# Performance work log

Hardware: AMD Instinct MI355X
Metric: run time of the kernel (lower is better)

The kernel has to match this reference:

```python
import jax, jax.numpy as jnp
import numpy as np

N, E, F, H, G, C = 50000, 800000, 128, 128, 500, 10
L = 3  # num_conv_layers
EPS = 1e-5


def batch_norm(x, g, b):
    # training-mode BatchNorm1d: biased variance, eps=1e-5
    mu = jnp.mean(x, axis=0)
    var = jnp.var(x, axis=0)
    return (x - mu) * jax.lax.rsqrt(var + EPS) * g + b


def gcn_conv(x, W, bias, src, dst, n):
    # x' = D^{-1/2} (A + I) D^{-1/2} (x W) + bias, edge weights = 1
    xw = x @ W
    loop = jnp.arange(n)
    s = jnp.concatenate([src, loop])  # sources incl. self-loops
    d = jnp.concatenate([dst, loop])  # targets incl. self-loops
    w = jnp.ones(s.shape[0], x.dtype)
    deg = jax.ops.segment_sum(w, s, num_segments=n)
    dinv = jnp.where(deg > 0, jax.lax.rsqrt(deg), 0.0)
    norm = dinv[s] * w * dinv[d]
    msg = xw[s] * norm[:, None]  # gather + scale
    out = jax.ops.segment_sum(msg, d, num_segments=n)  # scatter-add
    return out + bias


def setup_inputs() -> dict:
    key = jax.random.key(0)
    ks = jax.random.split(key, 16)
    x = jax.random.normal(ks[0], (N, F), dtype=jnp.float32)
    edge_index = jax.random.randint(ks[1], (2, E), 0, N, dtype=jnp.int64)
    batch = jnp.sort(jax.random.randint(ks[2], (N,), 0, G, dtype=jnp.int64))
    sF = 1.0 / np.sqrt(F)
    sH = 1.0 / np.sqrt(H)
    return {
        "x": x,
        "edge_index": edge_index,
        "batch": batch,
        "bn_feat_g": jnp.ones((F,), jnp.float32),
        "bn_feat_b": jnp.full((F,), 1e-4, jnp.float32),
        "W_feat": jax.random.normal(ks[3], (F, H), jnp.float32) * sF,
        "bns_conv_g": jnp.ones((L, H), jnp.float32),
        "bns_conv_b": jnp.full((L, H), 1e-4, jnp.float32),
        "W_conv": jax.random.normal(ks[4], (L, H, H), jnp.float32) * sH,
        "b_conv": jnp.zeros((L, H), jnp.float32),
        "bn_fc_g": jnp.ones((H,), jnp.float32),
        "bn_fc_b": jnp.full((H,), 1e-4, jnp.float32),
        "W_lin": jax.random.normal(ks[5], (H, H), jnp.float32) * sH,
        "b_lin": jnp.zeros((H,), jnp.float32),
        "bn_hid_g": jnp.ones((H,), jnp.float32),
        "bn_hid_b": jnp.full((H,), 1e-4, jnp.float32),
        "W_cls": jax.random.normal(ks[6], (H, C), jnp.float32) * sH,
        "b_cls": jnp.zeros((C,), jnp.float32),
    }


def reference(x, edge_index, batch, bn_feat_g, bn_feat_b, W_feat,
              bns_conv_g, bns_conv_b, W_conv, b_conv,
              bn_fc_g, bn_fc_b, W_lin, b_lin,
              bn_hid_g, bn_hid_b, W_cls, b_cls):
    src, dst = edge_index[0], edge_index[1]
    h = batch_norm(x, bn_feat_g, bn_feat_b)
    h = jax.nn.relu(h @ W_feat)  # gfn conv: linear only, no bias/propagation
    for i in range(L):
        h = batch_norm(h, bns_conv_g[i], bns_conv_b[i])
        h = jax.nn.relu(gcn_conv(h, W_conv[i], b_conv[i], src, dst, N))
    h = jax.ops.segment_sum(h, batch, num_segments=G)  # global_add_pool
    h = batch_norm(h, bn_fc_g, bn_fc_b)
    h = jax.nn.relu(h @ W_lin + b_lin)
    h = batch_norm(h, bn_hid_g, bn_hid_b)
    logits = h @ W_cls + b_cls
    return jax.nn.log_softmax(logits, axis=-1)
```

## Files before the change

### kernel.cpp

```cpp
#include <hip/hip_runtime.h>

#define NF 128
#define EPS 1e-5f
#define KELL 64
#define HB 64
#define HRANGE 32768
#define BCAP 5120
#define SB 512

typedef unsigned short ushort_t;
typedef unsigned int uint_t;

using bf16x8 = __attribute__((ext_vector_type(8))) short;
using f32x4  = __attribute__((ext_vector_type(4))) float;

static __device__ inline ushort_t f2bf(float f) {
    uint_t u = __float_as_uint(f);
    return (ushort_t)((u + 0x7fffu + ((u >> 16) & 1u)) >> 16);
}


__launch_bounds__(1024)
__global__ void k_prep(const int* __restrict__ ei, uint_t* __restrict__ gcnt,
                       uint_t* __restrict__ bedge, uint_t* __restrict__ hpart,
                       const float* __restrict__ W0, const float* __restrict__ W123,
                       ushort_t* __restrict__ Wp, const float* __restrict__ x,
                       float* __restrict__ stx, int E, int n) {
    __shared__ union {
        struct { uint_t cnt[256]; uint_t cur[256]; uint_t base[256]; } bk;
        uint_t h2[HRANGE / 2];
        struct { float ls[1024]; float lq[1024]; } st;
    } sh;
    const int blk = blockIdx.x;
    const int t = threadIdx.x;

    if (blk < 256) {
        if (t < 256) { sh.bk.cnt[t] = 0; sh.bk.cur[t] = 0; }
        __syncthreads();
        const int chunk = (E + 255) / 256;
        const int e0 = blk * chunk;
        const int e1 = min(e0 + chunk, E);
        for (int e = e0 + t; e < e1; e += 1024)
            atomicAdd(&sh.bk.cnt[ei[E + e] >> 8], 1);
        __syncthreads();
        if (t < 256) {
            uint_t c = sh.bk.cnt[t];
            sh.bk.base[t] = c ? atomicAdd(&gcnt[t], c) : 0u;
        }
        __syncthreads();
        for (int e = e0 + t; e < e1; e += 1024) {
            int s = ei[e], d = ei[E + e];
            int b = d >> 8;
            uint_t pos = sh.bk.base[b] + atomicAdd(&sh.bk.cur[b], 1);
            if (pos < BCAP)
                bedge[((size_t)b << 12) + ((size_t)b << 10) + pos] =
                    ((uint_t)(d & 255) << 16) | (uint_t)s;
        }
    } else if (blk < 320) {
        const int b = blk - 256;
#pragma unroll
        for (int p = 0; p < 2; ++p) {
            int base = p * HRANGE;
            for (int w = t; w < HRANGE / 2; w += 1024) sh.h2[w] = 0;
            __syncthreads();
            for (int e = b * 1024 + t; e < E; e += HB * 1024) {
                unsigned u = (unsigned)(ei[e] - base);
                if (u < HRANGE)
                    atomicAdd(&sh.h2[u >> 1], 1u << ((u & 1) << 4));
            }
            __syncthreads();
            uint_t* dst = hpart + ((size_t)(p * HB + b) << 14);
            for (int w = t; w < HRANGE / 2; w += 1024) dst[w] = sh.h2[w];
            __syncthreads();
        }
    } else if (blk < 322) {
#pragma unroll
        for (int kk = 0; kk < 4; ++kk) {
            int gidx = (blk - 320) * 4096 + kk * 1024 + t;
            int mat = gidx >> 11, idx = gidx & 2047;
            const float* W = (mat == 0) ? W0 : (W123 + (size_t)(mat - 1) * NF * NF);
            int lane = idx & 63, ct = (idx >> 6) & 7, kc = idx >> 9;
            int m = lane & 15, q = lane >> 4;
            ushort_t o[8];
#pragma unroll
            for (int j = 0; j < 8; ++j)
                o[j] = f2bf(W[(kc * 32 + q * 8 + j) * NF + ct * 16 + m]);
            *(uint4*)&Wp[(size_t)gidx * 8] = *(uint4*)o;
        }
    } else {
        const int b = blk - 322;
        const int j = t & 127;
        const int row8 = t >> 7;
        float s = 0.f, q = 0.f;
        for (int r = b * 8 + row8; r < n; r += SB * 8) {
            float v = x[(size_t)r * NF + j];
            s += v; q += v * v;
        }
        sh.st.ls[t] = s; sh.st.lq[t] = q;
        __syncthreads();
        if (t < 128) {
            float ss = 0.f, qq = 0.f;
#pragma unroll
            for (int k = 0; k < 8; ++k) {
                ss += sh.st.ls[t + k * 128];
                qq += sh.st.lq[t + k * 128];
            }
            atomicAdd(&stx[t], ss);
            atomicAdd(&stx[NF + t], qq);
        }
    }
}

__launch_bounds__(256)
__global__ void k_build(const uint_t* __restrict__ gcnt, const uint_t* __restrict__ bedge,
                        const uint_t* __restrict__ hpart, int* __restrict__ ucnt,
                        float* __restrict__ dinv, ushort_t* __restrict__ colx,
                        ushort_t* __restrict__ BbSent, int n) {
    __shared__ ushort_t ell[256][KELL];
    __shared__ uint_t lcnt[256];
    const int b = blockIdx.x, t = threadIdx.x;
    lcnt[t] = 0;
    __syncthreads();
    const int nb = min((int)gcnt[b], BCAP);
    const int node0 = b << 8;
    const uint_t* bsrc = bedge + ((size_t)b << 12) + ((size_t)b << 10);
    for (int e = t; e < nb; e += 256) {
        uint_t pk = bsrc[e];
        int dl = (pk >> 16) & 255;
        uint_t pos = atomicAdd(&lcnt[dl], 1);
        if (pos < KELL - 1) ell[dl][pos] = (ushort_t)(pk & 0xffffu);
    }
    __syncthreads();
    const int i = node0 + t;
    if (i < n) {
        int w = min((int)lcnt[t], KELL - 1);
        ell[t][w] = (ushort_t)i;
        int len = (w + 16) & ~15;
        for (int q = w + 1; q < len; ++q) ell[t][q] = (ushort_t)n;
        ucnt[i] = w;
        int p = i >> 15;
        int u = i & (HRANGE - 1);
        int wd = u >> 1, sh = (u & 1) << 4;
        const uint_t* basep = hpart + ((size_t)(p * HB) << 14) + wd;
        uint_t sum = 0;
#pragma unroll 8
        for (int bb = 0; bb < HB; ++bb) sum += basep[(size_t)bb << 14];
        sum = (sum >> sh) & 0xffffu;
        dinv[i] = rsqrtf((float)sum + 1.0f);
    }
    __syncthreads();
    int nrow = min(n - node0, 256);
    if (nrow > 0) {
        const uint4* src = (const uint4*)&ell[0][0];
        uint4* dst = (uint4*)&colx[(size_t)node0 * KELL];
        int lim = nrow * (KELL * 2 / 16);
        for (int wds = t; wds < lim; wds += 256) dst[wds] = src[wds];
    }
    if (b == 0 && t < 64)
        ((uint_t*)BbSent)[t] = 0;
}


__global__ void bn_stats_bf(const ushort_t* __restrict__ h, float* __restrict__ stats, int n) {
    int j = threadIdx.x & 127;
    int half = threadIdx.x >> 7;
    float s = 0.f, q = 0.f;
    for (int r = blockIdx.x * 2 + half; r < n; r += gridDim.x * 2) {
        float v = __uint_as_float((uint_t)h[(size_t)r * NF + j] << 16);
        s += v;
        q += v * v;
    }
    __shared__ float ls[256], lq[256];
    ls[threadIdx.x] = s; lq[threadIdx.x] = q;
    __syncthreads();
    if (threadIdx.x < 128) {
        atomicAdd(&stats[j], ls[threadIdx.x] + ls[threadIdx.x + 128]);
        atomicAdd(&stats[NF + j], lq[threadIdx.x] + lq[threadIdx.x + 128]);
    }
}


#define HSTRIDE 136

__launch_bounds__(512)
__global__ void gemm_mfma(const void* __restrict__ In, int inbf, const ushort_t* __restrict__ Wp,
                          const float* __restrict__ stats, const float* __restrict__ gW,
                          const float* __restrict__ bB, float inv_n,
                          const float* __restrict__ bias, const float* __restrict__ rowscale,
                          float* __restrict__ out, ushort_t* __restrict__ outb,
                          float* __restrict__ statsOut,
                          int nrows, int relu, int obf) {
    __shared__ union {
        ushort_t hs[64 * HSTRIDE];
        float    ob[32][132];
        ushort_t obu[64][136];
    } shu;
    __shared__ float acs[256];
    __shared__ float cs[128], cq[128];
    const int tid = threadIdx.x;
    const int rb = blockIdx.x * 64;

    if (tid < 128) {
        float mean = stats[tid] * inv_n;
        float var = stats[NF + tid] * inv_n - mean * mean;
        float rstd = rsqrtf(var + EPS);
        float a = gW[tid] * rstd;
        acs[tid] = a;
        acs[NF + tid] = bB[tid] - mean * a;
        cs[tid] = 0.f; cq[tid] = 0.f;
    }
    __syncthreads();
    const float4* ac4 = (const float4*)acs;

#pragma unroll
    for (int p = 0; p < 4; ++p) {
        int idx = p * 512 + tid;
        int r = idx >> 5, k4 = idx & 31;
        int gr = rb + r;
        float4 v = make_float4(0.f, 0.f, 0.f, 0.f);
        if (gr < nrows) {
            if (inbf) {
                uint2 u = *(const uint2*)((const ushort_t*)In + (size_t)gr * NF + k4 * 4);
                v.x = __uint_as_float(u.x << 16);
                v.y = __uint_as_float(u.x & 0xffff0000u);
                v.z = __uint_as_float(u.y << 16);
                v.w = __uint_as_float(u.y & 0xffff0000u);
            } else {
                v = *(const float4*)((const float*)In + (size_t)gr * NF + k4 * 4);
            }
        }
        float4 a4 = ac4[k4], c4 = ac4[32 + k4];
        ushort_t o[4];
        o[0] = f2bf(fmaf(v.x, a4.x, c4.x));
        o[1] = f2bf(fmaf(v.y, a4.y, c4.y));
        o[2] = f2bf(fmaf(v.z, a4.z, c4.z));
        o[3] = f2bf(fmaf(v.w, a4.w, c4.w));
        *(uint2*)&shu.hs[r * HSTRIDE + k4 * 4] = *(uint2*)o;
    }
    __syncthreads();

    const int wave = tid >> 6, lane = tid & 63;
    const int wr = wave & 3;
    const int wc = wave >> 2;
    const int m = lane & 15, q = lane >> 4;
    const ushort_t* arow = &shu.hs[(wr * 16 + m) * HSTRIDE];

    f32x4 acc[4];
#pragma unroll
    for (int ct = 0; ct < 4; ++ct) acc[ct] = (f32x4){0.f, 0.f, 0.f, 0.f};

#pragma unroll
    for (int kc = 0; kc < 4; ++kc) {
        bf16x8 af = *(const bf16x8*)&arow[kc * 32 + q * 8];
        const ushort_t* wp = Wp + kc * 4096 + (wc * 4) * 512 + lane * 8;
#pragma unroll
        for (int ct = 0; ct < 4; ++ct) {
            bf16x8 bfr = *(const bf16x8*)&wp[ct * 512];
            acc[ct] = __builtin_amdgcn_mfma_f32_16x16x32_bf16(af, bfr, acc[ct], 0, 0, 0);
        }
    }

    int grows[4]; float rsv[4]; bool gv[4];
#pragma unroll
    for (int r = 0; r < 4; ++r) {
        grows[r] = rb + wr * 16 + q * 4 + r;
        gv[r] = grows[r] < nrows;
        rsv[r] = (obf && rowscale && gv[r]) ? rowscale[grows[r]] : 1.0f;
    }

    if (statsOut) {
#pragma unroll
        for (int ct = 0; ct < 4; ++ct) {
            int col = (wc * 4 + ct) * 16 + m;
            float bcol = bias ? bias[col] : 0.f;
            float s = 0.f, qq = 0.f;
#pragma unroll
            for (int r = 0; r < 4; ++r) {
                if (gv[r]) {
                    float v = acc[ct][r] + bcol;
                    if (relu) v = fmaxf(v, 0.f);
                    s += v; qq += v * v;
                }
            }
            atomicAdd(&cs[col], s); atomicAdd(&cq[col], qq);
        }
    }

    __syncthreads();

    if (obf) {
#pragma unroll
        for (int ct = 0; ct < 4; ++ct) {
            int col = (wc * 4 + ct) * 16 + m;
            float bcol = bias ? bias[col] : 0.f;
#pragma unroll
            for (int r = 0; r < 4; ++r) {
                int row = wr * 16 + q * 4 + r;
                float v = acc[ct][r] + bcol;
                if (relu) v = fmaxf(v, 0.f);
                shu.obu[row][col] = f2bf(v * rsv[r]);
            }
        }
        __syncthreads();
#pragma unroll
        for (int i = 0; i < 2; ++i) {
            int idx = i * 512 + tid;
            int r = idx >> 4, c8 = idx & 15;
            int grow = rb + r;
            if (grow < nrows)
                *(uint4*)&outb[(size_t)grow * NF + c8 * 8] =
                    *(const uint4*)&shu.obu[r][c8 * 8];
        }
    } else {
#pragma unroll
        for (int h = 0; h < 2; ++h) {
            if ((wr >> 1) == h) {
#pragma unroll
                for (int ct = 0; ct < 4; ++ct) {
                    int col = (wc * 4 + ct) * 16 + m;
                    float bcol = bias ? bias[col] : 0.f;
#pragma unroll
                    for (int r = 0; r < 4; ++r) {
                        int row = (wr & 1) * 16 + q * 4 + r;
                        float v = acc[ct][r] + bcol;
                        if (relu) v = fmaxf(v, 0.f);
                        shu.ob[row][col] = v;
                    }
                }
            }
            __syncthreads();
#pragma unroll
            for (int i = 0; i < 2; ++i) {
                int idx = i * 512 + tid;
                int r = idx >> 5, c4 = idx & 31;
                int grow = rb + h * 32 + r;
                if (grow < nrows)
                    *(float4*)&out[(size_t)grow * NF + c4 * 4] =
                        *(const float4*)&shu.ob[r][c4 * 4];
            }
            __syncthreads();
        }
    }

    if (statsOut) {
        if (tid < 128) {
            atomicAdd(&statsOut[tid], cs[tid]);
            atomicAdd(&statsOut[NF + tid], cq[tid]);
        }
    }
}


__launch_bounds__(256)
__global__ void gemm_bn(const float* __restrict__ Hh, const float* __restrict__ W,
                        const float* __restrict__ stats, const float* __restrict__ gW,
                        const float* __restrict__ bB, float inv_n,
                        const float* __restrict__ bias,
                        float* __restrict__ out, float* __restrict__ statsOut,
                        int nrows, int relu) {
    __shared__ float hsb[64][133];
    __shared__ float acs[256];
    __shared__ float cs[128], cq[128];
    const int tid = threadIdx.x;
    const int tx = tid & 15;
    const int ty = tid >> 4;
    const int rb = blockIdx.x * 64;

    if (tid < 128) {
        float mean = stats[tid] * inv_n;
        float var = stats[NF + tid] * inv_n - mean * mean;
        float rstd = rsqrtf(var + EPS);
        float a = gW[tid] * rstd;
        acs[tid] = a;
        acs[NF + tid] = bB[tid] - mean * a;
        cs[tid] = 0.f; cq[tid] = 0.f;
    }
    __syncthreads();

#pragma unroll 8
    for (int p = 0; p < 32; ++p) {
        int idx = p * 256 + tid;
        int r = idx >> 7, k = idx & 127;
        int gr = rb + r;
        float v = (gr < nrows) ? Hh[(size_t)gr * NF + k] : 0.f;
        hsb[r][k] = fmaf(v, acs[k], acs[NF + k]);
    }
    __syncthreads();

    float acc[4][8];
#pragma unroll
    for (int i = 0; i < 4; ++i)
#pragma unroll
        for (int j = 0; j < 8; ++j) acc[i][j] = 0.f;

    const int c0 = tx * 4, c1 = 64 + tx * 4;
#pragma unroll 4
    for (int k = 0; k < 128; ++k) {
        const float4 b0 = *(const float4*)&W[k * NF + c0];
        const float4 b1 = *(const float4*)&W[k * NF + c1];
#pragma unroll
        for (int i = 0; i < 4; ++i) {
            float a = hsb[ty * 4 + i][k];
            acc[i][0] = fmaf(a, b0.x, acc[i][0]);
            acc[i][1] = fmaf(a, b0.y, acc[i][1]);
            acc[i][2] = fmaf(a, b0.z, acc[i][2]);
            acc[i][3] = fmaf(a, b0.w, acc[i][3]);
            acc[i][4] = fmaf(a, b1.x, acc[i][4]);
            acc[i][5] = fmaf(a, b1.y, acc[i][5]);
            acc[i][6] = fmaf(a, b1.z, acc[i][6]);
            acc[i][7] = fmaf(a, b1.w, acc[i][7]);
        }
    }

    float scol[8], qcol[8];
#pragma unroll
    for (int j = 0; j < 8; ++j) { scol[j] = 0.f; qcol[j] = 0.f; }
#pragma unroll
    for (int i = 0; i < 4; ++i) {
        int gr = rb + ty * 4 + i;
        if (gr < nrows) {
            float o[8];
#pragma unroll
            for (int j = 0; j < 8; ++j) {
                int c = (j < 4) ? (c0 + j) : (c1 + j - 4);
                float v = acc[i][j] + (bias ? bias[c] : 0.f);
                o[j] = relu ? fmaxf(v, 0.f) : v;
                scol[j] += o[j]; qcol[j] += o[j] * o[j];
            }
            *(float4*)&out[(size_t)gr * NF + c0] = make_float4(o[0], o[1], o[2], o[3]);
            *(float4*)&out[(size_t)gr * NF + c1] = make_float4(o[4], o[5], o[6], o[7]);
        }
    }
    if (statsOut) {
#pragma unroll
        for (int j = 0; j < 8; ++j) {
            int c = (j < 4) ? (c0 + j) : (c1 + j - 4);
            atomicAdd(&cs[c], scol[j]);
            atomicAdd(&cq[c], qcol[j]);
        }
        __syncthreads();
        if (tid < 128) {
            atomicAdd(&statsOut[tid], cs[tid]);
            atomicAdd(&statsOut[NF + tid], cq[tid]);
        }
    }
}


#define CVT2(u, a, b) { a = __uint_as_float((u) << 16); b = __uint_as_float((u) & 0xffff0000u); }
#define ACC8(q) { float p0, p1, p2, p3, p4, p5, p6, p7;                          \
    CVT2(q.x, p0, p1) CVT2(q.y, p2, p3) CVT2(q.z, p4, p5) CVT2(q.w, p6, p7)      \
    acc[0] += p0; acc[1] += p1; acc[2] += p2; acc[3] += p3;                      \
    acc[4] += p4; acc[5] += p5; acc[6] += p6; acc[7] += p7; }

__launch_bounds__(256)
__global__ void k_aggregate_bf(const ushort_t* __restrict__ xwb, const int* __restrict__ ucnt,
                               const ushort_t* __restrict__ colx, const float* __restrict__ dinv,
                               const float* __restrict__ bias, ushort_t* __restrict__ outb, int n) {
    int node = blockIdx.x * 16 + (threadIdx.x >> 4);
    int lane = threadIdx.x & 15;
    if (node >= n) return;
    const uint4* __restrict__ xq = (const uint4*)xwb;
    float acc[8];
#pragma unroll
    for (int j = 0; j < 8; ++j) acc[j] = 0.f;
    int dc = min(ucnt[node], KELL - 1);
    int len = (dc + 16) & ~15;
    int e0 = node * KELL;
    for (int e = e0; e < e0 + len; e += 16) {
        uint4 ia = *(const uint4*)&colx[e];
        uint4 ib = *(const uint4*)&colx[e + 8];
        int i0 = ia.x & 0xffff, i1 = ia.x >> 16;
        int i2 = ia.y & 0xffff, i3 = ia.y >> 16;
        int i4 = ia.z & 0xffff, i5 = ia.z >> 16;
        int i6 = ia.w & 0xffff, i7 = ia.w >> 16;
        int i8 = ib.x & 0xffff, i9 = ib.x >> 16;
        int iA = ib.y & 0xffff, iB = ib.y >> 16;
        int iC = ib.z & 0xffff, iD = ib.z >> 16;
        int iE = ib.w & 0xffff, iF = ib.w >> 16;
        uint4 q0 = xq[(size_t)i0 * 16 + lane];
        uint4 q1 = xq[(size_t)i1 * 16 + lane];
        uint4 q2 = xq[(size_t)i2 * 16 + lane];
        uint4 q3 = xq[(size_t)i3 * 16 + lane];
        uint4 q4 = xq[(size_t)i4 * 16 + lane];
        uint4 q5 = xq[(size_t)i5 * 16 + lane];
        uint4 q6 = xq[(size_t)i6 * 16 + lane];
        uint4 q7 = xq[(size_t)i7 * 16 + lane];
        uint4 q8 = xq[(size_t)i8 * 16 + lane];
        uint4 q9 = xq[(size_t)i9 * 16 + lane];
        uint4 qA = xq[(size_t)iA * 16 + lane];
        uint4 qB = xq[(size_t)iB * 16 + lane];
        uint4 qC = xq[(size_t)iC * 16 + lane];
        uint4 qD = xq[(size_t)iD * 16 + lane];
        uint4 qE = xq[(size_t)iE * 16 + lane];
        uint4 qF = xq[(size_t)iF * 16 + lane];
        ACC8(q0) ACC8(q1) ACC8(q2) ACC8(q3)
        ACC8(q4) ACC8(q5) ACC8(q6) ACC8(q7)
        ACC8(q8) ACC8(q9) ACC8(qA) ACC8(qB)
        ACC8(qC) ACC8(qD) ACC8(qE) ACC8(qF)
    }
    float di = dinv[node];
    float4 b0 = *(const float4*)&bias[lane * 8];
    float4 b1 = *(const float4*)&bias[lane * 8 + 4];
    float o[8];
    o[0] = fmaxf(fmaf(di, acc[0], b0.x), 0.f);
    o[1] = fmaxf(fmaf(di, acc[1], b0.y), 0.f);
    o[2] = fmaxf(fmaf(di, acc[2], b0.z), 0.f);
    o[3] = fmaxf(fmaf(di, acc[3], b0.w), 0.f);
    o[4] = fmaxf(fmaf(di, acc[4], b1.x), 0.f);
    o[5] = fmaxf(fmaf(di, acc[5], b1.y), 0.f);
    o[6] = fmaxf(fmaf(di, acc[6], b1.z), 0.f);
    o[7] = fmaxf(fmaf(di, acc[7], b1.w), 0.f);
    ushort_t ob[8];
#pragma unroll
    for (int j = 0; j < 8; ++j) ob[j] = f2bf(o[j]);
    *(uint4*)&outb[(size_t)node * NF + lane * 8] = *(uint4*)ob;
}


__global__ void k_pool_bf(const ushort_t* __restrict__ h, const int* __restrict__ batch,
                          float* __restrict__ pooled, float* __restrict__ stats, int n) {
    __shared__ float ps[8][128];
    int g = blockIdx.x;
    int t = threadIdx.x;
    int lane = t & 15;
    int rg = t >> 4;
    int lo = 0, hi = n;
    while (lo < hi) { int m = (lo + hi) >> 1; if (batch[m] < g) lo = m + 1; else hi = m; }
    int start = lo;
    lo = start; hi = n;
    while (lo < hi) { int m = (lo + hi) >> 1; if (batch[m] < g + 1) lo = m + 1; else hi = m; }
    int end = lo;
    float s[8];
#pragma unroll
    for (int j = 0; j < 8; ++j) s[j] = 0.f;
    for (int r = start + rg; r < end; r += 8) {
        uint4 u = *(const uint4*)&h[(size_t)r * NF + lane * 8];
        float p0, p1, p2, p3, p4, p5, p6, p7;
        CVT2(u.x, p0, p1) CVT2(u.y, p2, p3) CVT2(u.z, p4, p5) CVT2(u.w, p6, p7)
        s[0] += p0; s[1] += p1; s[2] += p2; s[3] += p3;
        s[4] += p4; s[5] += p5; s[6] += p6; s[7] += p7;
    }
#pragma unroll
    for (int j = 0; j < 8; ++j) ps[rg][lane * 8 + j] = s[j];
    __syncthreads();
    if (t < 128) {
        float v = 0.f;
#pragma unroll
        for (int k = 0; k < 8; ++k) v += ps[k][t];
        pooled[g * NF + t] = v;
        atomicAdd(&stats[t], v);
        atomicAdd(&stats[NF + t], v * v);
    }
}


__global__ void k_cls(const float* __restrict__ h, const float* __restrict__ stats,
                      const float* __restrict__ gW, const float* __restrict__ bB,
                      float inv_n, const float* __restrict__ Wc,
                      const float* __restrict__ bc, float* __restrict__ out, int C_) {
    __shared__ float hr[128];
    __shared__ float lg[16];
    __shared__ float lse_s;
    int r = blockIdx.x, t = threadIdx.x;
#pragma unroll
    for (int half = 0; half < 2; ++half) {
        int j = t + half * 64;
        float mean = stats[j] * inv_n;
        float var = stats[NF + j] * inv_n - mean * mean;
        float rstd = rsqrtf(var + EPS);
        float a = gW[j] * rstd;
        float c = bB[j] - mean * a;
        hr[j] = fmaf(h[r * NF + j], a, c);
    }
    __syncthreads();
    if (t < C_) {
        float s = bc[t];
        for (int k = 0; k < 128; ++k) s = fmaf(hr[k], Wc[k * C_ + t], s);
        lg[t] = s;
    }
    __syncthreads();
    if (t == 0) {
        float m = -1e30f;
        for (int c = 0; c < C_; ++c) m = fmaxf(m, lg[c]);
        float se = 0.f;
        for (int c = 0; c < C_; ++c) se += expf(lg[c] - m);
        lse_s = m + logf(se);
    }
    __syncthreads();
    if (t < C_) out[r * C_ + t] = lg[t] - lse_s;
}


extern "C" void kernel_launch(void* const* d_in, const int* in_sizes, int n_in,
                              void* d_out, int out_size, void* d_ws, size_t ws_size,
                              hipStream_t stream) {
    const float* x          = (const float*)d_in[0];
    const int*   ei         = (const int*)d_in[1];
    const int*   batch      = (const int*)d_in[2];
    const float* bn_feat_g  = (const float*)d_in[3];
    const float* bn_feat_b  = (const float*)d_in[4];
    const float* W_feat     = (const float*)d_in[5];
    const float* bns_conv_g = (const float*)d_in[6];
    const float* bns_conv_b = (const float*)d_in[7];
    const float* W_conv     = (const float*)d_in[8];
    const float* b_conv     = (const float*)d_in[9];
    const float* bn_fc_g    = (const float*)d_in[10];
    const float* bn_fc_b    = (const float*)d_in[11];
    const float* W_lin      = (const float*)d_in[12];
    const float* b_lin      = (const float*)d_in[13];
    const float* bn_hid_g   = (const float*)d_in[14];
    const float* bn_hid_b   = (const float*)d_in[15];
    const float* W_cls      = (const float*)d_in[16];
    const float* b_cls      = (const float*)d_in[17];
    float* outp = (float*)d_out;

    const int N_ = in_sizes[2];
    const int E_ = in_sizes[1] / 2;
    const int C_ = 10;
    const int G_ = out_size / C_;
    const int NBUCK = (N_ + 255) >> 8;

    char* wsp = (char*)d_ws;
    auto alloc = [&](size_t bytes) {
        void* p = (void*)wsp;
        wsp += (bytes + 255) & ~(size_t)255;
        return p;
    };
    uint_t*   gcnt   = (uint_t*)alloc(256 * 4);
    float*    statsA = (float*)alloc(6 * 256 * 4);
    ushort_t* Ab     = (ushort_t*)alloc((size_t)N_ * NF * 2);
    ushort_t* Bb     = (ushort_t*)alloc((size_t)(N_ + 1) * NF * 2);
    float*    dinv   = (float*)alloc((size_t)N_ * 4);
    int*      ucnt   = (int*)alloc((size_t)N_ * 4);
    uint_t*   bedge  = (uint_t*)alloc((size_t)256 * BCAP * 4);
    ushort_t* colx   = (ushort_t*)alloc((size_t)N_ * KELL * 2);
    uint_t*   hpart  = (uint_t*)alloc((size_t)2 * HB * (HRANGE / 2) * 4);
    ushort_t* Wp     = (ushort_t*)alloc((size_t)4 * NF * NF * 2);
    float*    pooled = (float*)alloc((size_t)G_ * NF * 4);
    float*    y2     = (float*)alloc((size_t)G_ * NF * 4);

    float* st_x  = statsA;
    float* st_f  = statsA + 256;
    float* st_a1 = statsA + 512;
    float* st_a2 = statsA + 768;
    float* st_pl = statsA + 1024;
    float* st_y2 = statsA + 1280;

    int nb_g = (N_ + 63) / 64;

    hipMemsetAsync(gcnt, 0, 1024 + 6 * 256 * 4, stream);

    k_prep<<<322 + SB, 1024, 0, stream>>>(ei, gcnt, bedge, hpart, W_feat, W_conv, Wp,
                                          x, st_x, E_, N_);
    k_build<<<NBUCK, 256, 0, stream>>>(gcnt, bedge, hpart, ucnt, dinv, colx,
                                       Bb + (size_t)N_ * NF, N_);

    gemm_mfma<<<nb_g, 512, 0, stream>>>(x, 0, Wp, st_x, bn_feat_g, bn_feat_b, 1.0f / N_,
                                        nullptr, nullptr, nullptr, Ab, st_f, N_, 1, 1);

    float* st_in[3] = {st_f, st_a1, st_a2};
    float* st_out[3] = {st_a1, st_a2, nullptr};
    for (int l = 0; l < 3; ++l) {
        gemm_mfma<<<nb_g, 512, 0, stream>>>(Ab, 1, Wp + (size_t)(l + 1) * NF * NF,
                                            st_in[l], bns_conv_g + l * NF, bns_conv_b + l * NF,
                                            1.0f / N_, nullptr, dinv, nullptr, Bb, nullptr,
                                            N_, 0, 1);
        k_aggregate_bf<<<(N_ + 15) / 16, 256, 0, stream>>>(Bb, ucnt, colx, dinv,
                                                           b_conv + l * NF, Ab, N_);
        if (st_out[l])
            bn_stats_bf<<<512, 256, 0, stream>>>(Ab, st_out[l], N_);
    }

    k_pool_bf<<<G_, 128, 0, stream>>>(Ab, batch, pooled, st_pl, N_);

    gemm_bn<<<(G_ + 63) / 64, 256, 0, stream>>>(pooled, W_lin, st_pl, bn_fc_g, bn_fc_b,
                                                1.0f / G_, b_lin, y2, st_y2, G_, 1);

    k_cls<<<G_, 64, 0, stream>>>(y2, st_y2, bn_hid_g, bn_hid_b, 1.0f / G_,
                                 W_cls, b_cls, outp, C_);
}
```

Baseline: 405.3 us.

## Fuse GCN layer kernels into one persistent cooperative kernel with grid syncs

Replaces the chain of per-layer GEMM, aggregation and BN-stats kernel launches with a single cooperative persistent kernel of 256 blocks. Stages are separated by grid-wide syncs, and the work is distributed with grid-stride loops over tiles and node groups. This is meant to remove launch gaps and tail effects between the many small kernels. The trade-off is reduced occupancy (one 512-thread block per CU, 256 blocks) and grid-sync overhead. A fallback non-cooperative path is kept in case the cooperative launch fails.

```diff
diff --git a/kernel.cpp b/kernel.cpp
--- a/kernel.cpp
+++ b/kernel.cpp
@@ -1,4 +1,7 @@
 #include <hip/hip_runtime.h>
+#include <hip/hip_cooperative_groups.h>
+
+namespace cg = cooperative_groups;
 
 #define NF 128
 #define EPS 1e-5f
@@ -7,6 +10,7 @@
 #define HRANGE 32768
 #define BCAP 5120
 #define SB 512
+#define CBLK 256
 
 typedef unsigned short ushort_t;
 typedef unsigned int uint_t;
@@ -161,56 +165,38 @@
 }
 
 
-__global__ void bn_stats_bf(const ushort_t* __restrict__ h, float* __restrict__ stats, int n) {
-    int j = threadIdx.x & 127;
-    int half = threadIdx.x >> 7;
-    float s = 0.f, q = 0.f;
-    for (int r = blockIdx.x * 2 + half; r < n; r += gridDim.x * 2) {
-        float v = __uint_as_float((uint_t)h[(size_t)r * NF + j] << 16);
-        s += v;
-        q += v * v;
-    }
-    __shared__ float ls[256], lq[256];
-    ls[threadIdx.x] = s; lq[threadIdx.x] = q;
-    __syncthreads();
-    if (threadIdx.x < 128) {
-        atomicAdd(&stats[j], ls[threadIdx.x] + ls[threadIdx.x + 128]);
-        atomicAdd(&stats[NF + j], lq[threadIdx.x] + lq[threadIdx.x + 128]);
-    }
-}
-
-
 #define HSTRIDE 136
 
-__launch_bounds__(512)
-__global__ void gemm_mfma(const void* __restrict__ In, int inbf, const ushort_t* __restrict__ Wp,
-                          const float* __restrict__ stats, const float* __restrict__ gW,
-                          const float* __restrict__ bB, float inv_n,
-                          const float* __restrict__ bias, const float* __restrict__ rowscale,
-                          float* __restrict__ out, ushort_t* __restrict__ outb,
-                          float* __restrict__ statsOut,
-                          int nrows, int relu, int obf) {
-    __shared__ union {
+struct SharedU {
+    union {
         ushort_t hs[64 * HSTRIDE];
-        float    ob[32][132];
         ushort_t obu[64][136];
-    } shu;
-    __shared__ float acs[256];
-    __shared__ float cs[128], cq[128];
+        struct { float ls[512]; float lq[512]; } st;
+    } u;
+    float acs[256];
+    float cs[128], cq[128];
+};
+
+static __device__ void gemm_tile(SharedU* sh, int tile, const void* In, int inbf,
+                                 const ushort_t* Wp, const float* stats,
+                                 const float* gW, const float* bB, float inv_n,
+                                 const float* rowscale, ushort_t* outb,
+                                 float* statsOut, int nrows, int relu) {
     const int tid = threadIdx.x;
-    const int rb = blockIdx.x * 64;
-
+    const int rb = tile * 64;
+
+    __syncthreads();
     if (tid < 128) {
         float mean = stats[tid] * inv_n;
         float var = stats[NF + tid] * inv_n - mean * mean;
         float rstd = rsqrtf(var + EPS);
         float a = gW[tid] * rstd;
-        acs[tid] = a;
-        acs[NF + tid] = bB[tid] - mean * a;
-        cs[tid] = 0.f; cq[tid] = 0.f;
-    }
-    __syncthreads();
-    const float4* ac4 = (const float4*)acs;
+        sh->acs[tid] = a;
+        sh->acs[NF + tid] = bB[tid] - mean * a;
+        if (statsOut) { sh->cs[tid] = 0.f; sh->cq[tid] = 0.f; }
+    }
+    __syncthreads();
+    const float4* ac4 = (const float4*)sh->acs;
 
 #pragma unroll
     for (int p = 0; p < 4; ++p) {
@@ -235,7 +221,7 @@
         o[1] = f2bf(fmaf(v.y, a4.y, c4.y));
         o[2] = f2bf(fmaf(v.z, a4.z, c4.z));
         o[3] = f2bf(fmaf(v.w, a4.w, c4.w));
-        *(uint2*)&shu.hs[r * HSTRIDE + k4 * 4] = *(uint2*)o;
+        *(uint2*)&sh->u.hs[r * HSTRIDE + k4 * 4] = *(uint2*)o;
     }
     __syncthreads();
 
@@ -243,7 +229,7 @@
     const int wr = wave & 3;
     const int wc = wave >> 2;
     const int m = lane & 15, q = lane >> 4;
-    const ushort_t* arow = &shu.hs[(wr * 16 + m) * HSTRIDE];
+    const ushort_t* arow = &sh->u.hs[(wr * 16 + m) * HSTRIDE];
 
     f32x4 acc[4];
 #pragma unroll
@@ -265,88 +251,245 @@
     for (int r = 0; r < 4; ++r) {
         grows[r] = rb + wr * 16 + q * 4 + r;
         gv[r] = grows[r] < nrows;
-        rsv[r] = (obf && rowscale && gv[r]) ? rowscale[grows[r]] : 1.0f;
+        rsv[r] = (rowscale && gv[r]) ? rowscale[grows[r]] : 1.0f;
     }
 
     if (statsOut) {
 #pragma unroll
         for (int ct = 0; ct < 4; ++ct) {
             int col = (wc * 4 + ct) * 16 + m;
-            float bcol = bias ? bias[col] : 0.f;
             float s = 0.f, qq = 0.f;
 #pragma unroll
             for (int r = 0; r < 4; ++r) {
                 if (gv[r]) {
-                    float v = acc[ct][r] + bcol;
+                    float v = acc[ct][r];
                     if (relu) v = fmaxf(v, 0.f);
                     s += v; qq += v * v;
                 }
             }
-            atomicAdd(&cs[col], s); atomicAdd(&cq[col], qq);
-        }
-    }
-
-    __syncthreads();
-
-    if (obf) {
-#pragma unroll
-        for (int ct = 0; ct < 4; ++ct) {
-            int col = (wc * 4 + ct) * 16 + m;
-            float bcol = bias ? bias[col] : 0.f;
-#pragma unroll
-            for (int r = 0; r < 4; ++r) {
-                int row = wr * 16 + q * 4 + r;
-                float v = acc[ct][r] + bcol;
-                if (relu) v = fmaxf(v, 0.f);
-                shu.obu[row][col] = f2bf(v * rsv[r]);
-            }
-        }
-        __syncthreads();
-#pragma unroll
-        for (int i = 0; i < 2; ++i) {
-            int idx = i * 512 + tid;
-            int r = idx >> 4, c8 = idx & 15;
-            int grow = rb + r;
-            if (grow < nrows)
-                *(uint4*)&outb[(size_t)grow * NF + c8 * 8] =
-                    *(const uint4*)&shu.obu[r][c8 * 8];
-        }
-    } else {
-#pragma unroll
-        for (int h = 0; h < 2; ++h) {
-            if ((wr >> 1) == h) {
-#pragma unroll
-                for (int ct = 0; ct < 4; ++ct) {
-                    int col = (wc * 4 + ct) * 16 + m;
-                    float bcol = bias ? bias[col] : 0.f;
-#pragma unroll
-                    for (int r = 0; r < 4; ++r) {
-                        int row = (wr & 1) * 16 + q * 4 + r;
-                        float v = acc[ct][r] + bcol;
-                        if (relu) v = fmaxf(v, 0.f);
-                        shu.ob[row][col] = v;
-                    }
-                }
-            }
-            __syncthreads();
-#pragma unroll
-            for (int i = 0; i < 2; ++i) {
-                int idx = i * 512 + tid;
-                int r = idx >> 5, c4 = idx & 31;
-                int grow = rb + h * 32 + r;
-                if (grow < nrows)
-                    *(float4*)&out[(size_t)grow * NF + c4 * 4] =
-                        *(const float4*)&shu.ob[r][c4 * 4];
-            }
-            __syncthreads();
-        }
-    }
-
+            atomicAdd(&sh->cs[col], s); atomicAdd(&sh->cq[col], qq);
+        }
+    }
+
+    __syncthreads();
+
+#pragma unroll
+    for (int ct = 0; ct < 4; ++ct) {
+        int col = (wc * 4 + ct) * 16 + m;
+#pragma unroll
+        for (int r = 0; r < 4; ++r) {
+            int row = wr * 16 + q * 4 + r;
+            float v = acc[ct][r];
+            if (relu) v = fmaxf(v, 0.f);
+            sh->u.obu[row][col] = f2bf(v * rsv[r]);
+        }
+    }
+    __syncthreads();
+#pragma unroll
+    for (int i = 0; i < 2; ++i) {
+        int idx = i * 512 + tid;
+        int r = idx >> 4, c8 = idx & 15;
+        int grow = rb + r;
+        if (grow < nrows)
+            *(uint4*)&outb[(size_t)grow * NF + c8 * 8] =
+                *(const uint4*)&sh->u.obu[r][c8 * 8];
+    }
     if (statsOut) {
         if (tid < 128) {
-            atomicAdd(&statsOut[tid], cs[tid]);
-            atomicAdd(&statsOut[NF + tid], cq[tid]);
-        }
+            atomicAdd(&statsOut[tid], sh->cs[tid]);
+            atomicAdd(&statsOut[NF + tid], sh->cq[tid]);
+        }
+    }
+}
+
+#define CVT2(u, a, b) { a = __uint_as_float((u) << 16); b = __uint_as_float((u) & 0xffff0000u); }
+#define ACC8(q) { float p0, p1, p2, p3, p4, p5, p6, p7;                          \
+    CVT2(q.x, p0, p1) CVT2(q.y, p2, p3) CVT2(q.z, p4, p5) CVT2(q.w, p6, p7)      \
+    acc[0] += p0; acc[1] += p1; acc[2] += p2; acc[3] += p3;                      \
+    acc[4] += p4; acc[5] += p5; acc[6] += p6; acc[7] += p7; }
+
+static __device__ void agg32(int base, const ushort_t* xwb, const int* ucnt,
+                             const ushort_t* colx, const float* dinv,
+                             const float* bias, ushort_t* outb, int n) {
+    int node = base + (threadIdx.x >> 4);
+    int lane = threadIdx.x & 15;
+    if (node < n) {
+        const uint4* xq = (const uint4*)xwb;
+        float acc[8];
+#pragma unroll
+        for (int j = 0; j < 8; ++j) acc[j] = 0.f;
+        int dc = min(ucnt[node], KELL - 1);
+        int len = (dc + 16) & ~15;
+        int e0 = node * KELL;
+        for (int e = e0; e < e0 + len; e += 16) {
+            uint4 ia = *(const uint4*)&colx[e];
+            uint4 ib = *(const uint4*)&colx[e + 8];
+            int i0 = ia.x & 0xffff, i1 = ia.x >> 16;
+            int i2 = ia.y & 0xffff, i3 = ia.y >> 16;
+            int i4 = ia.z & 0xffff, i5 = ia.z >> 16;
+            int i6 = ia.w & 0xffff, i7 = ia.w >> 16;
+            int i8 = ib.x & 0xffff, i9 = ib.x >> 16;
+            int iA = ib.y & 0xffff, iB = ib.y >> 16;
+            int iC = ib.z & 0xffff, iD = ib.z >> 16;
+            int iE = ib.w & 0xffff, iF = ib.w >> 16;
+            uint4 q0 = xq[(size_t)i0 * 16 + lane];
+            uint4 q1 = xq[(size_t)i1 * 16 + lane];
+            uint4 q2 = xq[(size_t)i2 * 16 + lane];
+            uint4 q3 = xq[(size_t)i3 * 16 + lane];
+            uint4 q4 = xq[(size_t)i4 * 16 + lane];
+            uint4 q5 = xq[(size_t)i5 * 16 + lane];
+            uint4 q6 = xq[(size_t)i6 * 16 + lane];
+            uint4 q7 = xq[(size_t)i7 * 16 + lane];
+            uint4 q8 = xq[(size_t)i8 * 16 + lane];
+            uint4 q9 = xq[(size_t)i9 * 16 + lane];
+            uint4 qA = xq[(size_t)iA * 16 + lane];
+            uint4 qB = xq[(size_t)iB * 16 + lane];
+            uint4 qC = xq[(size_t)iC * 16 + lane];
+            uint4 qD = xq[(size_t)iD * 16 + lane];
+            uint4 qE = xq[(size_t)iE * 16 + lane];
+            uint4 qF = xq[(size_t)iF * 16 + lane];
+            ACC8(q0) ACC8(q1) ACC8(q2) ACC8(q3)
+            ACC8(q4) ACC8(q5) ACC8(q6) ACC8(q7)
+            ACC8(q8) ACC8(q9) ACC8(qA) ACC8(qB)
+            ACC8(qC) ACC8(qD) ACC8(qE) ACC8(qF)
+        }
+        float di = dinv[node];
+        float4 b0 = *(const float4*)&bias[lane * 8];
+        float4 b1 = *(const float4*)&bias[lane * 8 + 4];
+        float o[8];
+        o[0] = fmaxf(fmaf(di, acc[0], b0.x), 0.f);
+        o[1] = fmaxf(fmaf(di, acc[1], b0.y), 0.f);
+        o[2] = fmaxf(fmaf(di, acc[2], b0.z), 0.f);
+        o[3] = fmaxf(fmaf(di, acc[3], b0.w), 0.f);
+        o[4] = fmaxf(fmaf(di, acc[4], b1.x), 0.f);
+        o[5] = fmaxf(fmaf(di, acc[5], b1.y), 0.f);
+        o[6] = fmaxf(fmaf(di, acc[6], b1.z), 0.f);
+        o[7] = fmaxf(fmaf(di, acc[7], b1.w), 0.f);
+        ushort_t ob[8];
+#pragma unroll
+        for (int j = 0; j < 8; ++j) ob[j] = f2bf(o[j]);
+        *(uint4*)&outb[(size_t)node * NF + lane * 8] = *(uint4*)ob;
+    }
+}
+
+static __device__ void stats_ab(SharedU* sh, const ushort_t* h, float* statsOut, int n) {
+    const int t = threadIdx.x;
+    int j = t & 127, rq = t >> 7;
+    float s = 0.f, q = 0.f;
+    for (int r = blockIdx.x * 4 + rq; r < n; r += gridDim.x * 4) {
+        float v = __uint_as_float((uint_t)h[(size_t)r * NF + j] << 16);
+        s += v; q += v * v;
+    }
+    __syncthreads();
+    sh->u.st.ls[t] = s; sh->u.st.lq[t] = q;
+    __syncthreads();
+    if (t < 128) {
+        float ss = sh->u.st.ls[t] + sh->u.st.ls[t + 128] + sh->u.st.ls[t + 256] + sh->u.st.ls[t + 384];
+        float qq = sh->u.st.lq[t] + sh->u.st.lq[t + 128] + sh->u.st.lq[t + 256] + sh->u.st.lq[t + 384];
+        atomicAdd(&statsOut[j], ss);
+        atomicAdd(&statsOut[NF + j], qq);
+    }
+}
+
+
+__launch_bounds__(512)
+__global__ void k_core(const float* __restrict__ x, const ushort_t* __restrict__ Wp,
+                       float* __restrict__ statsA,
+                       const float* __restrict__ bn_feat_g, const float* __restrict__ bn_feat_b,
+                       const float* __restrict__ bns_conv_g, const float* __restrict__ bns_conv_b,
+                       const float* __restrict__ b_conv, const float* __restrict__ dinv,
+                       const int* __restrict__ ucnt, const ushort_t* __restrict__ colx,
+                       ushort_t* __restrict__ Ab, ushort_t* __restrict__ Bb, int n) {
+    __shared__ SharedU sh;
+    cg::grid_group grid = cg::this_grid();
+    const float inv_n = 1.0f / n;
+    const int ntile = (n + 63) >> 6;
+    const int ngrp = (n + 31) >> 5;
+
+#define GSYNC() { __threadfence(); grid.sync(); __threadfence(); }
+
+    for (int tile = blockIdx.x; tile < ntile; tile += gridDim.x)
+        gemm_tile(&sh, tile, x, 0, Wp, statsA , bn_feat_g, bn_feat_b, inv_n,
+                  nullptr, Ab, statsA + 256 , n, 1);
+    GSYNC();
+
+    for (int l = 0; l < 3; ++l) {
+        const float* st_in = statsA + 256 + l * 256;
+        for (int tile = blockIdx.x; tile < ntile; tile += gridDim.x)
+            gemm_tile(&sh, tile, Ab, 1, Wp + (size_t)(l + 1) * NF * NF, st_in,
+                      bns_conv_g + l * NF, bns_conv_b + l * NF, inv_n,
+                      dinv, Bb, nullptr, n, 0);
+        GSYNC();
+        for (int g = blockIdx.x; g < ngrp; g += gridDim.x)
+            agg32(g << 5, Bb, ucnt, colx, dinv, b_conv + l * NF, Ab, n);
+        GSYNC();
+        if (l < 2) {
+            stats_ab(&sh, Ab, statsA + 512 + l * 256, n);
+            GSYNC();
+        }
+    }
+#undef GSYNC
+}
+
+
+__launch_bounds__(512)
+__global__ void k_gemm1(const void* __restrict__ In, int inbf, const ushort_t* __restrict__ Wp,
+                        const float* __restrict__ stats, const float* __restrict__ gW,
+                        const float* __restrict__ bB, float inv_n,
+                        const float* __restrict__ rowscale, ushort_t* __restrict__ outb,
+                        float* __restrict__ statsOut, int nrows, int relu) {
+    __shared__ SharedU sh;
+    gemm_tile(&sh, blockIdx.x, In, inbf, Wp, stats, gW, bB, inv_n, rowscale, outb,
+              statsOut, nrows, relu);
+}
+
+__launch_bounds__(512)
+__global__ void k_agg1(const ushort_t* __restrict__ xwb, const int* __restrict__ ucnt,
+                       const ushort_t* __restrict__ colx, const float* __restrict__ dinv,
+                       const float* __restrict__ bias, ushort_t* __restrict__ outb, int n) {
+    agg32(blockIdx.x << 5, xwb, ucnt, colx, dinv, bias, outb, n);
+}
+
+__launch_bounds__(512)
+__global__ void k_stats1(const ushort_t* __restrict__ h, float* __restrict__ statsOut, int n) {
+    __shared__ SharedU sh;
+    stats_ab(&sh, h, statsOut, n);
+}
+
+
+__global__ void k_pool_bf(const ushort_t* __restrict__ h, const int* __restrict__ batch,
+                          float* __restrict__ pooled, float* __restrict__ stats, int n) {
+    __shared__ float ps[8][128];
+    int g = blockIdx.x;
+    int t = threadIdx.x;
+    int lane = t & 15;
+    int rg = t >> 4;
+    int lo = 0, hi = n;
+    while (lo < hi) { int m = (lo + hi) >> 1; if (batch[m] < g) lo = m + 1; else hi = m; }
+    int start = lo;
+    lo = start; hi = n;
+    while (lo < hi) { int m = (lo + hi) >> 1; if (batch[m] < g + 1) lo = m + 1; else hi = m; }
+    int end = lo;
+    float s[8];
+#pragma unroll
+    for (int j = 0; j < 8; ++j) s[j] = 0.f;
+    for (int r = start + rg; r < end; r += 8) {
+        uint4 u = *(const uint4*)&h[(size_t)r * NF + lane * 8];
+        float p0, p1, p2, p3, p4, p5, p6, p7;
+        CVT2(u.x, p0, p1) CVT2(u.y, p2, p3) CVT2(u.z, p4, p5) CVT2(u.w, p6, p7)
+        s[0] += p0; s[1] += p1; s[2] += p2; s[3] += p3;
+        s[4] += p4; s[5] += p5; s[6] += p6; s[7] += p7;
+    }
+#pragma unroll
+    for (int j = 0; j < 8; ++j) ps[rg][lane * 8 + j] = s[j];
+    __syncthreads();
+    if (t < 128) {
+        float v = 0.f;
+#pragma unroll
+        for (int k = 0; k < 8; ++k) v += ps[k][t];
+        pooled[g * NF + t] = v;
+        atomicAdd(&stats[t], v);
+        atomicAdd(&stats[NF + t], v * v);
     }
 }
 
@@ -443,114 +586,6 @@
             atomicAdd(&statsOut[tid], cs[tid]);
             atomicAdd(&statsOut[NF + tid], cq[tid]);
         }
-    }
-}
-
-
-#define CVT2(u, a, b) { a = __uint_as_float((u) << 16); b = __uint_as_float((u) & 0xffff0000u); }
-#define ACC8(q) { float p0, p1, p2, p3, p4, p5, p6, p7;                          \
-    CVT2(q.x, p0, p1) CVT2(q.y, p2, p3) CVT2(q.z, p4, p5) CVT2(q.w, p6, p7)      \
-    acc[0] += p0; acc[1] += p1; acc[2] += p2; acc[3] += p3;                      \
-    acc[4] += p4; acc[5] += p5; acc[6] += p6; acc[7] += p7; }
-
-__launch_bounds__(256)
-__global__ void k_aggregate_bf(const ushort_t* __restrict__ xwb, const int* __restrict__ ucnt,
-                               const ushort_t* __restrict__ colx, const float* __restrict__ dinv,
-                               const float* __restrict__ bias, ushort_t* __restrict__ outb, int n) {
-    int node = blockIdx.x * 16 + (threadIdx.x >> 4);
-    int lane = threadIdx.x & 15;
-    if (node >= n) return;
-    const uint4* __restrict__ xq = (const uint4*)xwb;
-    float acc[8];
-#pragma unroll
-    for (int j = 0; j < 8; ++j) acc[j] = 0.f;
-    int dc = min(ucnt[node], KELL - 1);
-    int len = (dc + 16) & ~15;
-    int e0 = node * KELL;
-    for (int e = e0; e < e0 + len; e += 16) {
-        uint4 ia = *(const uint4*)&colx[e];
-        uint4 ib = *(const uint4*)&colx[e + 8];
-        int i0 = ia.x & 0xffff, i1 = ia.x >> 16;
-        int i2 = ia.y & 0xffff, i3 = ia.y >> 16;
-        int i4 = ia.z & 0xffff, i5 = ia.z >> 16;
-        int i6 = ia.w & 0xffff, i7 = ia.w >> 16;
-        int i8 = ib.x & 0xffff, i9 = ib.x >> 16;
-        int iA = ib.y & 0xffff, iB = ib.y >> 16;
-        int iC = ib.z & 0xffff, iD = ib.z >> 16;
-        int iE = ib.w & 0xffff, iF = ib.w >> 16;
-        uint4 q0 = xq[(size_t)i0 * 16 + lane];
-        uint4 q1 = xq[(size_t)i1 * 16 + lane];
-        uint4 q2 = xq[(size_t)i2 * 16 + lane];
-        uint4 q3 = xq[(size_t)i3 * 16 + lane];
-        uint4 q4 = xq[(size_t)i4 * 16 + lane];
-        uint4 q5 = xq[(size_t)i5 * 16 + lane];
-        uint4 q6 = xq[(size_t)i6 * 16 + lane];
-        uint4 q7 = xq[(size_t)i7 * 16 + lane];
-        uint4 q8 = xq[(size_t)i8 * 16 + lane];
-        uint4 q9 = xq[(size_t)i9 * 16 + lane];
-        uint4 qA = xq[(size_t)iA * 16 + lane];
-        uint4 qB = xq[(size_t)iB * 16 + lane];
-        uint4 qC = xq[(size_t)iC * 16 + lane];
-        uint4 qD = xq[(size_t)iD * 16 + lane];
-        uint4 qE = xq[(size_t)iE * 16 + lane];
-        uint4 qF = xq[(size_t)iF * 16 + lane];
-        ACC8(q0) ACC8(q1) ACC8(q2) ACC8(q3)
-        ACC8(q4) ACC8(q5) ACC8(q6) ACC8(q7)
-        ACC8(q8) ACC8(q9) ACC8(qA) ACC8(qB)
-        ACC8(qC) ACC8(qD) ACC8(qE) ACC8(qF)
-    }
-    float di = dinv[node];
-    float4 b0 = *(const float4*)&bias[lane * 8];
-    float4 b1 = *(const float4*)&bias[lane * 8 + 4];
-    float o[8];
-    o[0] = fmaxf(fmaf(di, acc[0], b0.x), 0.f);
-    o[1] = fmaxf(fmaf(di, acc[1], b0.y), 0.f);
-    o[2] = fmaxf(fmaf(di, acc[2], b0.z), 0.f);
-    o[3] = fmaxf(fmaf(di, acc[3], b0.w), 0.f);
-    o[4] = fmaxf(fmaf(di, acc[4], b1.x), 0.f);
-    o[5] = fmaxf(fmaf(di, acc[5], b1.y), 0.f);
-    o[6] = fmaxf(fmaf(di, acc[6], b1.z), 0.f);
-    o[7] = fmaxf(fmaf(di, acc[7], b1.w), 0.f);
-    ushort_t ob[8];
-#pragma unroll
-    for (int j = 0; j < 8; ++j) ob[j] = f2bf(o[j]);
-    *(uint4*)&outb[(size_t)node * NF + lane * 8] = *(uint4*)ob;
-}
-
-
-__global__ void k_pool_bf(const ushort_t* __restrict__ h, const int* __restrict__ batch,
-                          float* __restrict__ pooled, float* __restrict__ stats, int n) {
-    __shared__ float ps[8][128];
-    int g = blockIdx.x;
-    int t = threadIdx.x;
-    int lane = t & 15;
-    int rg = t >> 4;
-    int lo = 0, hi = n;
-    while (lo < hi) { int m = (lo + hi) >> 1; if (batch[m] < g) lo = m + 1; else hi = m; }
-    int start = lo;
-    lo = start; hi = n;
-    while (lo < hi) { int m = (lo + hi) >> 1; if (batch[m] < g + 1) lo = m + 1; else hi = m; }
-    int end = lo;
-    float s[8];
-#pragma unroll
-    for (int j = 0; j < 8; ++j) s[j] = 0.f;
-    for (int r = start + rg; r < end; r += 8) {
-        uint4 u = *(const uint4*)&h[(size_t)r * NF + lane * 8];
-        float p0, p1, p2, p3, p4, p5, p6, p7;
-        CVT2(u.x, p0, p1) CVT2(u.y, p2, p3) CVT2(u.z, p4, p5) CVT2(u.w, p6, p7)
-        s[0] += p0; s[1] += p1; s[2] += p2; s[3] += p3;
-        s[4] += p4; s[5] += p5; s[6] += p6; s[7] += p7;
-    }
-#pragma unroll
-    for (int j = 0; j < 8; ++j) ps[rg][lane * 8 + j] = s[j];
-    __syncthreads();
-    if (t < 128) {
-        float v = 0.f;
-#pragma unroll
-        for (int k = 0; k < 8; ++k) v += ps[k][t];
-        pooled[g * NF + t] = v;
-        atomicAdd(&stats[t], v);
-        atomicAdd(&stats[NF + t], v * v);
     }
 }
 
@@ -647,7 +682,8 @@
     float* st_pl = statsA + 1024;
     float* st_y2 = statsA + 1280;
 
-    int nb_g = (N_ + 63) / 64;
+    const int nb_g = (N_ + 63) / 64;
+    const float inv_n = 1.0f / N_;
 
     hipMemsetAsync(gcnt, 0, 1024 + 6 * 256 * 4, stream);
 
@@ -656,20 +692,32 @@
     k_build<<<NBUCK, 256, 0, stream>>>(gcnt, bedge, hpart, ucnt, dinv, colx,
                                        Bb + (size_t)N_ * NF, N_);
 
-    gemm_mfma<<<nb_g, 512, 0, stream>>>(x, 0, Wp, st_x, bn_feat_g, bn_feat_b, 1.0f / N_,
-                                        nullptr, nullptr, nullptr, Ab, st_f, N_, 1, 1);
-
-    float* st_in[3] = {st_f, st_a1, st_a2};
-    float* st_out[3] = {st_a1, st_a2, nullptr};
-    for (int l = 0; l < 3; ++l) {
-        gemm_mfma<<<nb_g, 512, 0, stream>>>(Ab, 1, Wp + (size_t)(l + 1) * NF * NF,
-                                            st_in[l], bns_conv_g + l * NF, bns_conv_b + l * NF,
-                                            1.0f / N_, nullptr, dinv, nullptr, Bb, nullptr,
-                                            N_, 0, 1);
-        k_aggregate_bf<<<(N_ + 15) / 16, 256, 0, stream>>>(Bb, ucnt, colx, dinv,
-                                                           b_conv + l * NF, Ab, N_);
-        if (st_out[l])
-            bn_stats_bf<<<512, 256, 0, stream>>>(Ab, st_out[l], N_);
+    hipError_t ce;
+    {
+        void* ka[] = {(void*)&x, (void*)&Wp, (void*)&statsA,
+                      (void*)&bn_feat_g, (void*)&bn_feat_b,
+                      (void*)&bns_conv_g, (void*)&bns_conv_b, (void*)&b_conv,
+                      (void*)&dinv, (void*)&ucnt, (void*)&colx,
+                      (void*)&Ab, (void*)&Bb, (void*)&N_};
+        ce = hipLaunchCooperativeKernel((const void*)k_core, dim3(CBLK), dim3(512),
+                                        ka, 0, stream);
+    }
+    if (ce != hipSuccess) {
+        (void)hipGetLastError();
+        k_gemm1<<<nb_g, 512, 0, stream>>>(x, 0, Wp, st_x, bn_feat_g, bn_feat_b, inv_n,
+                                          nullptr, Ab, st_f, N_, 1);
+        float* st_in[3] = {st_f, st_a1, st_a2};
+        float* st_out[3] = {st_a1, st_a2, nullptr};
+        for (int l = 0; l < 3; ++l) {
+            k_gemm1<<<nb_g, 512, 0, stream>>>(Ab, 1, Wp + (size_t)(l + 1) * NF * NF,
+                                              st_in[l], bns_conv_g + l * NF,
+                                              bns_conv_b + l * NF, inv_n,
+                                              dinv, Bb, nullptr, N_, 0);
+            k_agg1<<<(N_ + 31) / 32, 512, 0, stream>>>(Bb, ucnt, colx, dinv,
+                                                       b_conv + l * NF, Ab, N_);
+            if (st_out[l])
+                k_stats1<<<512, 512, 0, stream>>>(Ab, st_out[l], N_);
+        }
     }
 
     k_pool_bf<<<G_, 128, 0, stream>>>(Ab, batch, pooled, st_pl, N_);
```

Result: slower. 1.352 ms (+233.6%).
